# Kernel optimization log

Hardware: AMD Instinct MI355X
Metric: run time of the kernel (lower is better)

## Reference

```python
import jax, jax.numpy as jnp
import numpy as np
from jax import lax

# ---- Haar (db1) wavelet filters, matching create_wavelet_filter ----
_S2 = float(1.0 / np.sqrt(2.0))
_dec_lo = np.array([_S2, _S2], np.float32)    # pywt dec_lo reversed (symmetric)
_dec_hi = np.array([_S2, -_S2], np.float32)   # pywt dec_hi [-s,s] reversed
_rec_lo = np.array([_S2, _S2], np.float32)    # pywt rec_lo flipped (symmetric)
_rec_hi = np.array([-_S2, _S2], np.float32)   # pywt rec_hi [s,-s] flipped

def _outer(a, b):  # torch: a.unsqueeze(0) * b.unsqueeze(1) -> [i,j] = a[j]*b[i]
    return b[:, None] * a[None, :]

DEC = jnp.asarray(np.stack([_outer(_dec_lo, _dec_lo), _outer(_dec_lo, _dec_hi),
                            _outer(_dec_hi, _dec_lo), _outer(_dec_hi, _dec_hi)]))  # [4,2,2]
REC = jnp.asarray(np.stack([_outer(_rec_lo, _rec_lo), _outer(_rec_lo, _rec_hi),
                            _outer(_rec_hi, _rec_lo), _outer(_rec_hi, _rec_hi)]))  # [4,2,2]

BN_EPS = 1e-5

def mish(x):
    return x * jnp.tanh(jax.nn.softplus(x))

def silu(x):
    return x * jax.nn.sigmoid(x)

def bn(x, g, b):  # eval-mode BatchNorm2d with running_mean=0, running_var=1
    return x * (g / jnp.sqrt(1.0 + BN_EPS))[None, :, None, None] + b[None, :, None, None]

def dwconv(x, w, pad):  # depthwise conv, w: [C,1,k,k]
    return lax.conv_general_dilated(x, w, (1, 1), [(pad, pad), (pad, pad)],
                                    feature_group_count=x.shape[1],
                                    dimension_numbers=('NCHW', 'OIHW', 'NCHW'))

def dyn_dwconv(x, ew, gw):
    # DynamicConv2d (depthwise experts). ew: [E,C,1,k,k], gw: [E,C]
    gates = jax.nn.softmax(x.mean((2, 3)) @ gw.T, axis=-1)  # [B,E]
    k = ew.shape[-1]
    outs = jnp.stack([dwconv(x, ew[e], k // 2) for e in range(ew.shape[0])], 1)  # [B,E,C,H,W]
    return jnp.einsum('be,bechw->bchw', gates, outs)

def local_branch(x, ew, gw, bn1g, bn1b, pw, bn2g, bn2b):
    # DWConv2d_BN_ReLU: dynamic dwconv -> BN -> Mish -> depthwise 1x1 (per-channel scale) -> BN
    y = mish(bn(dyn_dwconv(x, ew, gw), bn1g, bn1b))
    y = y * pw[None, :, None, None]
    return bn(y, bn2g, bn2b)

def sel_scan(u, xw, dtw, dtb, Alog, Dp):
    # u: [B,L,D]; xw: [R+2N,D]; dtw: [D,R]; dtb: [D]; Alog: [D,N]; Dp: [D]
    R = dtw.shape[1]
    N = Alog.shape[1]
    xdbl = jnp.einsum('bld,ed->ble', u, xw)
    dt, Bm, Cm = xdbl[..., :R], xdbl[..., R:R + N], xdbl[..., R + N:]
    delta = jax.nn.softplus(jnp.einsum('blr,dr->bld', dt, dtw) + dtb)  # [B,L,D]
    A = -jnp.exp(Alog)                                                  # [D,N]
    a = jnp.exp(delta[..., None] * A)                                   # [B,L,D,N]
    b = delta[..., None] * Bm[:, :, None, :] * u[..., None]             # [B,L,D,N]
    def comb(c1, c2):
        a1, b1 = c1
        a2, b2 = c2
        return a1 * a2, a2 * b1 + b2
    _, h = lax.associative_scan(comb, (a, b), axis=1)                    # h_t = a_t h_{t-1} + b_t
    return jnp.einsum('bldn,bln->bld', h, Cm) + Dp * u

def ss2d(x, in_w, cw, cb, xpw, dtw, dtb, Alog, Dp, ow):
    # SS2D (d_state=1, k_group=2, channel_first): in_proj -> dwconv+silu -> 2-direction
    # selective scan -> gate with silu(z) -> out_proj.
    B, C, H, W = x.shape
    xz = jnp.einsum('oc,bchw->bohw', in_w, x)
    d = in_w.shape[0] // 2
    xi, z = xz[:, :d], xz[:, d:]
    xc = silu(dwconv(xi, cw, 1) + cb[None, :, None, None])
    u0 = xc.reshape(B, d, H * W).transpose(0, 2, 1)                       # row-major scan
    u1 = xc.transpose(0, 1, 3, 2).reshape(B, d, H * W).transpose(0, 2, 1)  # col-major scan
    y0 = sel_scan(u0, xpw[0], dtw[0], dtb[0], Alog[0], Dp[0])
    y1 = sel_scan(u1, xpw[1], dtw[1], dtb[1], Alog[1], Dp[1])
    y0 = y0.transpose(0, 2, 1).reshape(B, d, H, W)
    y1 = y1.transpose(0, 2, 1).reshape(B, d, W, H).transpose(0, 1, 3, 2)
    y = (y0 + y1) * silu(z)
    return jnp.einsum('oc,bchw->bohw', ow, y)

def mbwt(x, wav_w, wav_b, wav_scale, base_scale,
         ss_in_w, ss_conv_w, ss_conv_b, ss_xproj_w, ss_dt_w, ss_dt_b, ss_A_log, ss_D, ss_out_w):
    # MBWTConv2d, wt_levels=1, H/W even. Haar WT (2x2 stride 2) == block reshape + einsum.
    B, C, H, W = x.shape
    xr = x.reshape(B, C, H // 2, 2, W // 2, 2)
    wt = jnp.einsum('bchpwq,kpq->bckhw', xr, DEC)                  # [B,C,4,h,w]
    tag = wt.reshape(B, 4 * C, H // 2, W // 2)
    tag = dwconv(tag, wav_w, wav_w.shape[-1] // 2) + wav_b[None, :, None, None]
    tag = (tag * wav_scale).reshape(B, C, 4, H // 2, W // 2)
    # inverse Haar WT (conv_transpose 2x2 stride 2, groups=C)
    up = jnp.einsum('bckhw,kpq->bchpwq', tag, REC).reshape(B, C, H, W)
    g = ss2d(x, ss_in_w, ss_conv_w, ss_conv_b, ss_xproj_w, ss_dt_w, ss_dt_b, ss_A_log, ss_D, ss_out_w)
    return base_scale * g + up


def setup_inputs() -> dict:
    key = jax.random.key(0)
    ks = iter(jax.random.split(key, 64))
    B, DIM, H, W = 16, 256, 64, 64
    Cg = Cl = 64
    d = {'x': jax.random.normal(next(ks), (B, DIM, H, W), jnp.float32)}
    for j, k in enumerate((3, 5, 7)):
        p = f'l{j}_'
        d[p + 'ew'] = jax.random.normal(next(ks), (4, Cl, 1, k, k), jnp.float32) * 0.1
        d[p + 'gw'] = jax.random.normal(next(ks), (4, Cl), jnp.float32) * 0.1
        d[p + 'bn1g'] = jnp.ones((Cl,), jnp.float32)
        d[p + 'bn1b'] = jnp.zeros((Cl,), jnp.float32)
        d[p + 'pw'] = jax.random.normal(next(ks), (Cl,), jnp.float32) * 0.2
        d[p + 'bn2g'] = jnp.ones((Cl,), jnp.float32)
        d[p + 'bn2b'] = jnp.zeros((Cl,), jnp.float32)
    d['wav_w'] = jax.random.normal(next(ks), (4 * Cg, 1, 3, 3), jnp.float32) * 0.1
    d['wav_b'] = jnp.zeros((4 * Cg,), jnp.float32)
    d['wav_scale'] = jnp.full((1, 4 * Cg, 1, 1), 0.1, jnp.float32)
    d['base_scale'] = jnp.ones((1, Cg, 1, 1), jnp.float32)
    dm, R, N, K = Cg, 4, 1, 2  # d_inner, dt_rank, d_state, k_group
    d['ss_in_w'] = jax.random.normal(next(ks), (2 * dm, Cg), jnp.float32) * float(1 / np.sqrt(Cg))
    d['ss_conv_w'] = jax.random.normal(next(ks), (dm, 1, 3, 3), jnp.float32) * 0.1
    d['ss_conv_b'] = jnp.zeros((dm,), jnp.float32)
    d['ss_xproj_w'] = jax.random.normal(next(ks), (K, R + 2 * N, dm), jnp.float32) * float(1 / np.sqrt(dm))
    d['ss_dt_w'] = jax.random.normal(next(ks), (K, dm, R), jnp.float32) * float(1 / np.sqrt(R))
    d['ss_dt_b'] = jnp.full((K, dm), -2.0, jnp.float32)
    d['ss_A_log'] = jnp.zeros((K, dm, N), jnp.float32)
    d['ss_D'] = jnp.ones((K, dm), jnp.float32)
    d['ss_out_w'] = jax.random.normal(next(ks), (Cg, dm), jnp.float32) * float(1 / np.sqrt(dm))
    return d


def reference(x,
              l0_ew, l0_gw, l0_bn1g, l0_bn1b, l0_pw, l0_bn2g, l0_bn2b,
              l1_ew, l1_gw, l1_bn1g, l1_bn1b, l1_pw, l1_bn2g, l1_bn2b,
              l2_ew, l2_gw, l2_bn1g, l2_bn1b, l2_pw, l2_bn2g, l2_bn2b,
              wav_w, wav_b, wav_scale, base_scale,
              ss_in_w, ss_conv_w, ss_conv_b, ss_xproj_w, ss_dt_w, ss_dt_b, ss_A_log, ss_D, ss_out_w):
    Cg, Cl = 64, 64
    xg, xl, xi = x[:, :Cg], x[:, Cg:Cg + Cl], x[:, Cg + Cl:]
    yl = (local_branch(xl, l0_ew, l0_gw, l0_bn1g, l0_bn1b, l0_pw, l0_bn2g, l0_bn2b)
          + local_branch(xl, l1_ew, l1_gw, l1_bn1g, l1_bn1b, l1_pw, l1_bn2g, l1_bn2b)
          + local_branch(xl, l2_ew, l2_gw, l2_bn1g, l2_bn1b, l2_pw, l2_bn2g, l2_bn2b))
    yg = mbwt(xg, wav_w, wav_b, wav_scale, base_scale,
              ss_in_w, ss_conv_w, ss_conv_b, ss_xproj_w, ss_dt_w, ss_dt_b, ss_A_log, ss_D, ss_out_w)
    return jnp.concatenate([yg, yl, xi], axis=1)
```

## Files before the change

### kernel.cpp

```cpp
#include <hip/hip_runtime.h>
#include <math.h>

static constexpr int NB   = 16;
static constexpr int DIM  = 256;
static constexpr int CG   = 64;
static constexpr int HH   = 64;
static constexpr int WW   = 64;
static constexpr int HW   = HH * WW;

__device__ __forceinline__ float mish_fast(float x) {
    float t = __expf(fminf(x, 20.f));
    float p = __builtin_fmaf(t, t, t + t);
    return x * p * __builtin_amdgcn_rcpf(p + 2.f);
}
__device__ __forceinline__ float silu_f(float x) {
    return x * __builtin_amdgcn_rcpf(1.f + __expf(-x));
}
__device__ __forceinline__ float softplus_fast(float x) {
    return fmaxf(x, 0.f) + __logf(1.f + __expf(-fabsf(x)));
}

__global__ __launch_bounds__(256) void k_stage1(
    const float* __restrict__ x,
    const float* __restrict__ wav_w, const float* __restrict__ wav_b,
    const float* __restrict__ wav_scale,
    float* __restrict__ up, float* __restrict__ mean,
    const float* __restrict__ in_w,
    float* __restrict__ xi, float* __restrict__ z) {
    __shared__ float smem[8640];
    int bid = blockIdx.x;
    int tid = threadIdx.x;

    if (bid < 1024) {
        int c = bid & 63, b = bid >> 6;
        float* xs  = smem;
        float* wtb = smem + 4160;
        float* red = smem + 8384;
        const float* xp = x + ((size_t)b * DIM + c) * HW;
        for (int i = tid; i < HW; i += 256) xs[(i >> 6) * 65 + (i & 63)] = xp[i];
        {
            const float* lp = x + ((size_t)b * DIM + 64 + c) * HW;
            float s = 0.f;
            for (int i = tid; i < HW; i += 256) s += lp[i];
            red[tid] = s;
            __syncthreads();
            for (int o = 128; o > 0; o >>= 1) {
                if (tid < o) red[tid] += red[tid + o];
                __syncthreads();
            }
            if (tid == 0) mean[b * 64 + c] = red[0] * (1.f / HW);
        }
        for (int i = tid; i < 1024; i += 256) {
            int h = i >> 5, w = i & 31;
            float a  = xs[(2 * h) * 65 + 2 * w],     bb = xs[(2 * h) * 65 + 2 * w + 1];
            float cc = xs[(2 * h + 1) * 65 + 2 * w], dd = xs[(2 * h + 1) * 65 + 2 * w + 1];
            wtb[0 * 1056 + h * 33 + w] = 0.5f * (a + bb + cc + dd);
            wtb[1 * 1056 + h * 33 + w] = 0.5f * (a + bb - cc - dd);
            wtb[2 * 1056 + h * 33 + w] = 0.5f * (a - bb + cc - dd);
            wtb[3 * 1056 + h * 33 + w] = 0.5f * (a - bb - cc + dd);
        }
        __syncthreads();
        float wk[4][9], tb[4];
#pragma unroll
        for (int k = 0; k < 4; ++k) {
            int ch = c * 4 + k;
            float sc = wav_scale[ch];
#pragma unroll
            for (int j = 0; j < 9; ++j) wk[k][j] = wav_w[ch * 9 + j] * sc;
            tb[k] = wav_b[ch] * sc;
        }
        float* upp = up + ((size_t)b * CG + c) * HW;
        for (int i = tid; i < 1024; i += 256) {
            int h = i >> 5, w = i & 31;
            float tg[4];
#pragma unroll
            for (int k = 0; k < 4; ++k) {
                float s = tb[k];
#pragma unroll
                for (int dy = -1; dy <= 1; ++dy) {
                    int hh = h + dy;
                    if (hh < 0 || hh >= 32) continue;
#pragma unroll
                    for (int dx = -1; dx <= 1; ++dx) {
                        int wx = w + dx;
                        if (wx < 0 || wx >= 32) continue;
                        s = fmaf(wtb[k * 1056 + hh * 33 + wx], wk[k][(dy + 1) * 3 + (dx + 1)], s);
                    }
                }
                tg[k] = s;
            }
            float u00 = 0.5f * (tg[0] - tg[1] - tg[2] + tg[3]);
            float u01 = 0.5f * (tg[0] - tg[1] + tg[2] - tg[3]);
            float u10 = 0.5f * (tg[0] + tg[1] - tg[2] - tg[3]);
            float u11 = 0.5f * (tg[0] + tg[1] + tg[2] + tg[3]);
            upp[(2 * h) * 64 + 2 * w]         = u00;
            upp[(2 * h) * 64 + 2 * w + 1]     = u01;
            upp[(2 * h + 1) * 64 + 2 * w]     = u10;
            upp[(2 * h + 1) * 64 + 2 * w + 1] = u11;
        }
    } else {
        int id2 = bid - 1024;
        int h0 = (id2 & 31) * 2;
        int b  = id2 >> 5;
        float* xs = smem;
        float* wt = smem + 4096;

        float acc[8][8];
#pragma unroll
        for (int i = 0; i < 8; ++i)
#pragma unroll
            for (int j = 0; j < 8; ++j) acc[i][j] = 0.f;

        int o0 = (tid >> 4) * 8;
        int p0 = (tid & 15) * 8;

        for (int ko = 0; ko < 64; ko += 32) {
            if (ko) __syncthreads();
            {
                int s = tid;
#pragma unroll
                for (int it = 0; it < 4; ++it, s += 256) {
                    int c = s >> 5, p4 = (s & 31) * 4;
                    float4 v = *(const float4*)(x + ((size_t)b * DIM + ko + c) * HW + h0 * 64 + p4);
                    *(float4*)(xs + c * 128 + p4) = v;
                }
            }
            {
                int s = tid;
#pragma unroll
                for (int it = 0; it < 4; ++it, s += 256) {
                    int o = s >> 3, c0 = (s & 7) * 4;
                    float4 v = *(const float4*)(in_w + o * 64 + ko + c0);
                    wt[(c0 + 0) * 128 + o] = v.x;
                    wt[(c0 + 1) * 128 + o] = v.y;
                    wt[(c0 + 2) * 128 + o] = v.z;
                    wt[(c0 + 3) * 128 + o] = v.w;
                }
            }
            __syncthreads();
#pragma unroll 4
            for (int c = 0; c < 32; ++c) {
                float xv[8], wv[8];
                *(float4*)(xv)     = *(const float4*)(xs + c * 128 + p0);
                *(float4*)(xv + 4) = *(const float4*)(xs + c * 128 + p0 + 4);
                *(float4*)(wv)     = *(const float4*)(wt + c * 128 + o0);
                *(float4*)(wv + 4) = *(const float4*)(wt + c * 128 + o0 + 4);
#pragma unroll
                for (int i = 0; i < 8; ++i)
#pragma unroll
                    for (int j = 0; j < 8; ++j)
                        acc[i][j] = fmaf(wv[i], xv[j], acc[i][j]);
            }
        }

#pragma unroll
        for (int i = 0; i < 8; ++i) {
            int o = o0 + i;
            float* dst = (o < 64) ? (xi + ((size_t)b * 64 + o) * HW + h0 * 64)
                                  : (z + ((size_t)b * 64 + (o - 64)) * HW + h0 * 64);
            *(float4*)(dst + p0)     = make_float4(acc[i][0], acc[i][1], acc[i][2], acc[i][3]);
            *(float4*)(dst + p0 + 4) = make_float4(acc[i][4], acc[i][5], acc[i][6], acc[i][7]);
        }
    }
}

__global__ __launch_bounds__(256) void k_stage2(
    const float* __restrict__ xi,
    const float* __restrict__ cw, const float* __restrict__ cb,
    const float* __restrict__ xpw,
    float* __restrict__ xc, float4* __restrict__ proj4, float2* __restrict__ projBC,
    const float* __restrict__ mean,
    const float* __restrict__ ew3, const float* __restrict__ gw3, const float* __restrict__ g13,
    const float* __restrict__ ew5, const float* __restrict__ gw5, const float* __restrict__ g15,
    const float* __restrict__ ew7, const float* __restrict__ gw7, const float* __restrict__ g17,
    float* __restrict__ w3o, float* __restrict__ w5o, float* __restrict__ w7o) {
    __shared__ float smem[12608];
    int bid = blockIdx.x;
    int tid = threadIdx.x;

    if (bid < 512) {
        int h0 = (bid & 31) * 2;
        int b  = bid >> 5;
        float* xs  = smem;
        float* xcs = smem + 8448;

        int dir = tid >> 7;
        int px  = tid & 127;
        float acc0 = 0.f, acc1 = 0.f, acc2 = 0.f, acc3 = 0.f, acc4 = 0.f, acc5 = 0.f;

        int cl_c = tid >> 3;
        int p0_c = (tid & 7) * 16;
        int row_c = p0_c >> 6;
        int wb_c  = p0_c & 63;

        for (int ch0 = 0; ch0 < 64; ch0 += 32) {
            if (ch0) __syncthreads();
            {
                int s = tid;
#pragma unroll
                for (int it = 0; it < 8; ++it, s += 256) {
                    int c = s >> 6;
                    int rem = s & 63;
                    int r = rem >> 4, w4 = (rem & 15) * 4;
                    int gh = h0 - 1 + r;
                    float4 v = make_float4(0.f, 0.f, 0.f, 0.f);
                    if (gh >= 0 && gh < 64)
                        v = *(const float4*)(xi + ((size_t)b * 64 + ch0 + c) * HW + gh * 64 + w4);
                    float* dp = xs + c * 264 + r * 66 + 1 + w4;
                    dp[0] = v.x; dp[1] = v.y; dp[2] = v.z; dp[3] = v.w;
                }
                if (tid < 128) {
                    int cl = tid >> 2, r = tid & 3;
                    xs[cl * 264 + r * 66 + 0]  = 0.f;
                    xs[cl * 264 + r * 66 + 65] = 0.f;
                }
            }
            __syncthreads();

            {
                float wk[9];
#pragma unroll
                for (int j = 0; j < 9; ++j) wk[j] = cw[(ch0 + cl_c) * 9 + j];
                float bias = cb[ch0 + cl_c];
                float accr[16];
#pragma unroll
                for (int k = 0; k < 16; ++k) accr[k] = bias;
#pragma unroll
                for (int dy = 0; dy < 3; ++dy) {
                    const float* rp = xs + cl_c * 264 + (row_c + dy) * 66 + wb_c;
                    float r[18];
#pragma unroll
                    for (int q = 0; q < 18; ++q) r[q] = rp[q];
#pragma unroll
                    for (int k = 0; k < 16; ++k)
#pragma unroll
                        for (int dx = 0; dx < 3; ++dx)
                            accr[k] = fmaf(r[k + dx], wk[dy * 3 + dx], accr[k]);
                }
#pragma unroll
                for (int k = 0; k < 16; ++k)
                    xcs[cl_c * 130 + p0_c + k] = silu_f(accr[k]);
            }
            __syncthreads();

            {
                int s = tid;
#pragma unroll
                for (int it = 0; it < 4; ++it, s += 256) {
                    int c = s >> 5, pq = (s & 31) * 4;
                    const float* sp = xcs + c * 130 + pq;
                    *(float4*)(xc + ((size_t)b * 64 + ch0 + c) * HW + h0 * 64 + pq) =
                        make_float4(sp[0], sp[1], sp[2], sp[3]);
                }
            }
            {
                const float* wp = xpw + dir * 6 * 64 + ch0;
#pragma unroll 8
                for (int c = 0; c < 32; ++c) {
                    float xv = xcs[c * 130 + px];
                    acc0 = fmaf(xv, wp[0 * 64 + c], acc0);
                    acc1 = fmaf(xv, wp[1 * 64 + c], acc1);
                    acc2 = fmaf(xv, wp[2 * 64 + c], acc2);
                    acc3 = fmaf(xv, wp[3 * 64 + c], acc3);
                    acc4 = fmaf(xv, wp[4 * 64 + c], acc4);
                    acc5 = fmaf(xv, wp[5 * 64 + c], acc5);
                }
            }
        }

        int h = h0 + (px >> 6), w = px & 63;
        int l = (dir == 0) ? (h * 64 + w) : (w * 64 + h);
        size_t base = ((size_t)dir * NB + b) * HW + l;
        proj4[base]  = make_float4(acc0, acc1, acc2, acc3);
        projBC[base] = make_float2(acc4, acc5);
    } else {
        int b = bid - 512;
        int c = tid;
        float* m = smem;
        float* g = smem + 64;
        if (c < 64) m[c] = mean[b * 64 + c];
        __syncthreads();
        const float rs = rsqrtf(1.f + 1e-5f);

#define WEFF_SECT(GW, EW, G1, OUT, K2)                                        \
        {                                                                     \
            if (c < 4) {                                                      \
                float l = 0.f;                                                \
                for (int cc = 0; cc < 64; ++cc) l += m[cc] * GW[c * 64 + cc]; \
                g[c] = l;                                                     \
            }                                                                 \
            __syncthreads();                                                  \
            if (c == 0) {                                                     \
                float mx = fmaxf(fmaxf(g[0], g[1]), fmaxf(g[2], g[3]));       \
                float e0 = expf(g[0] - mx), e1 = expf(g[1] - mx);             \
                float e2 = expf(g[2] - mx), e3 = expf(g[3] - mx);             \
                float inv = 1.f / (e0 + e1 + e2 + e3);                        \
                g[0] = e0 * inv; g[1] = e1 * inv; g[2] = e2 * inv; g[3] = e3 * inv; \
            }                                                                 \
            __syncthreads();                                                  \
            if (c < 64) {                                                     \
                float g1s = G1[c] * rs;                                       \
                for (int kk = 0; kk < K2; ++kk) {                             \
                    float w = 0.f;                                            \
                    for (int e = 0; e < 4; ++e) w += g[e] * EW[(e * 64 + c) * K2 + kk]; \
                    OUT[(b * 64 + c) * K2 + kk] = w * g1s;                    \
                }                                                             \
            }                                                                 \
            __syncthreads();                                                  \
        }

        WEFF_SECT(gw3, ew3, g13, w3o, 9)
        WEFF_SECT(gw5, ew5, g15, w5o, 25)
        WEFF_SECT(gw7, ew7, g17, w7o, 49)
#undef WEFF_SECT
    }
}

__global__ __launch_bounds__(256) void k_scan2(const float* __restrict__ xc,
                                               const float4* __restrict__ proj4,
                                               const float2* __restrict__ projBC,
                                               const float* __restrict__ dt_w,
                                               const float* __restrict__ dt_b,
                                               const float* __restrict__ A_log,
                                               const float* __restrict__ Dp,
                                               const float* __restrict__ z,
                                               float* __restrict__ yz) {
    int wave = threadIdx.x >> 6;
    int lane = threadIdx.x & 63;
    int wid = blockIdx.x;
    int b = wid >> 6;
    int d = wid & 63;

    __shared__ float ut[64 * 65];
    __shared__ float al[4][1088];
    __shared__ float bl[4][1088];
    __shared__ float aggA[4], aggB[4];

    const float* uplane = xc + ((size_t)b * 64 + d) * HW;
    const float4* up4 = (const float4*)uplane;
#pragma unroll
    for (int q = 0; q < 4; ++q) {
        int s = q * 256 + threadIdx.x;
        float4 v = up4[s];
        int r = s >> 4, c0 = (s & 15) * 4;
        float* p = ut + r * 65 + c0;
        p[0] = v.x; p[1] = v.y; p[2] = v.z; p[3] = v.w;
    }
    __syncthreads();

    int ch = wave;
    float* a_my = al[wave];
    float* b_my = bl[wave];
    float y0r[16];

    {
        float4 wv = *(const float4*)(dt_w + d * 4);
        float db = dt_b[d];
        float A = -__expf(A_log[d]);
        float Dv = Dp[d];
        const float4* p4 = proj4 + (size_t)b * HW;
        const float2* pBC = projBC + (size_t)b * HW;

        float uv[16], cm[16];
#pragma unroll
        for (int j = 0; j < 16; ++j) {
            int el = j * 64 + lane;
            int e  = ch * 1024 + el;
            float4 t4 = p4[e];
            float2 t2 = pBC[e];
            float u = ut[(ch * 16 + j) * 65 + lane];
            uv[j] = u; cm[j] = t2.y;
            float pre = fmaf(t4.x, wv.x, fmaf(t4.y, wv.y,
                        fmaf(t4.z, wv.z, fmaf(t4.w, wv.w, db))));
            float delta = softplus_fast(pre);
            float aj = __expf(delta * A);
            float bj = delta * t2.x * u;
            int idx = (el >> 4) * 17 + (el & 15);
            a_my[idx] = aj;
            b_my[idx] = bj;
        }
        __builtin_amdgcn_wave_barrier();

        float a[16], bb[16];
#pragma unroll
        for (int j = 0; j < 16; ++j) {
            a[j]  = a_my[lane * 17 + j];
            bb[j] = b_my[lane * 17 + j];
        }
        float As = 1.f, Bs = 0.f;
#pragma unroll
        for (int j = 0; j < 16; ++j) { Bs = fmaf(a[j], Bs, bb[j]); As *= a[j]; }
        float Ai = As, Bi = Bs;
#pragma unroll
        for (int off = 1; off < 64; off <<= 1) {
            float ap = __shfl_up(Ai, (unsigned)off, 64);
            float bp = __shfl_up(Bi, (unsigned)off, 64);
            if (lane >= off) { Bi = fmaf(Ai, bp, Bi); Ai *= ap; }
        }
        if (lane == 63) { aggA[wave] = Ai; aggB[wave] = Bi; }
        __syncthreads();
        float carry = 0.f;
        for (int k = 0; k < wave; ++k) carry = fmaf(aggA[k], carry, aggB[k]);
        float ap1 = __shfl_up(Ai, 1, 64);
        float bp1 = __shfl_up(Bi, 1, 64);
        float h = (lane == 0) ? carry : fmaf(ap1, carry, bp1);
#pragma unroll
        for (int j = 0; j < 16; ++j) {
            h = fmaf(a[j], h, bb[j]);
            a_my[lane * 17 + j] = h;
        }
        __builtin_amdgcn_wave_barrier();
#pragma unroll
        for (int j = 0; j < 16; ++j) {
            int el = j * 64 + lane;
            float hv = a_my[(el >> 4) * 17 + (el & 15)];
            y0r[j] = fmaf(hv, cm[j], Dv * uv[j]);
        }
    }
    __syncthreads();

    {
        int pd = 64 + d;
        float4 wv = *(const float4*)(dt_w + pd * 4);
        float db = dt_b[pd];
        float A = -__expf(A_log[pd]);
        float Dv = Dp[pd];
        const float4* p4 = proj4 + ((size_t)NB + b) * HW;
        const float2* pBC = projBC + ((size_t)NB + b) * HW;

        float uv[16], cm[16];
#pragma unroll
        for (int j = 0; j < 16; ++j) {
            int el = j * 64 + lane;
            int e  = ch * 1024 + el;
            float4 t4 = p4[e];
            float2 t2 = pBC[e];
            float u = ut[lane * 65 + (ch * 16 + j)];
            uv[j] = u; cm[j] = t2.y;
            float pre = fmaf(t4.x, wv.x, fmaf(t4.y, wv.y,
                        fmaf(t4.z, wv.z, fmaf(t4.w, wv.w, db))));
            float delta = softplus_fast(pre);
            float aj = __expf(delta * A);
            float bj = delta * t2.x * u;
            int idx = (el >> 4) * 17 + (el & 15);
            a_my[idx] = aj;
            b_my[idx] = bj;
        }
        __builtin_amdgcn_wave_barrier();

        float a[16], bb[16];
#pragma unroll
        for (int j = 0; j < 16; ++j) {
            a[j]  = a_my[lane * 17 + j];
            bb[j] = b_my[lane * 17 + j];
        }
        float As = 1.f, Bs = 0.f;
#pragma unroll
        for (int j = 0; j < 16; ++j) { Bs = fmaf(a[j], Bs, bb[j]); As *= a[j]; }
        float Ai = As, Bi = Bs;
#pragma unroll
        for (int off = 1; off < 64; off <<= 1) {
            float ap = __shfl_up(Ai, (unsigned)off, 64);
            float bp = __shfl_up(Bi, (unsigned)off, 64);
            if (lane >= off) { Bi = fmaf(Ai, bp, Bi); Ai *= ap; }
        }
        if (lane == 63) { aggA[wave] = Ai; aggB[wave] = Bi; }
        __syncthreads();
        float carry = 0.f;
        for (int k = 0; k < wave; ++k) carry = fmaf(aggA[k], carry, aggB[k]);
        float ap1 = __shfl_up(Ai, 1, 64);
        float bp1 = __shfl_up(Bi, 1, 64);
        float h = (lane == 0) ? carry : fmaf(ap1, carry, bp1);
#pragma unroll
        for (int j = 0; j < 16; ++j) {
            h = fmaf(a[j], h, bb[j]);
            a_my[lane * 17 + j] = h;
        }
        __builtin_amdgcn_wave_barrier();
#pragma unroll
        for (int j = 0; j < 16; ++j) {
            int el = j * 64 + lane;
            float hv = a_my[(el >> 4) * 17 + (el & 15)];
            ut[lane * 65 + (ch * 16 + j)] = fmaf(hv, cm[j], Dv * uv[j]);
        }
    }
    __syncthreads();

    const float* zp = z + ((size_t)b * 64 + d) * HW;
    float* yp = yz + ((size_t)b * 64 + d) * HW;
#pragma unroll
    for (int j = 0; j < 16; ++j) {
        int e = ch * 1024 + j * 64 + lane;
        float y1v = ut[(ch * 16 + j) * 65 + lane];
        float zz = zp[e];
        yp[e] = (y0r[j] + y1v) * silu_f(zz);
    }
}

__global__ __launch_bounds__(256) void k_stage4(
    const float* __restrict__ x,
    const float* __restrict__ w3, const float* __restrict__ w5, const float* __restrict__ w7,
    const float* __restrict__ b1_0, const float* __restrict__ pw0,
    const float* __restrict__ g2_0, const float* __restrict__ b2_0,
    const float* __restrict__ b1_1, const float* __restrict__ pw1,
    const float* __restrict__ g2_1, const float* __restrict__ b2_1,
    const float* __restrict__ b1_2, const float* __restrict__ pw2,
    const float* __restrict__ g2_2, const float* __restrict__ b2_2,
    const float* __restrict__ yz, const float* __restrict__ ow,
    const float* __restrict__ base_scale, const float* __restrict__ up,
    float* __restrict__ out) {
    __shared__ float smem[6144];
    int bid = blockIdx.x;
    int tid = threadIdx.x;

    if (bid < 4096) {
        int tile = bid & 3;
        int c = (bid >> 2) & 63;
        int b = bid >> 8;
        int oy = (tile >> 1) * 32, ox = (tile & 1) * 32;
        float* t = smem;
        const float* xp = x + ((size_t)b * DIM + 64 + c) * HW;
        for (int i = tid; i < 38 * 38; i += 256) {
            int r = i / 38, cc = i % 38;
            int yy = r - 3 + oy, xx = cc - 3 + ox;
            t[r * 40 + cc] = (yy >= 0 && yy < 64 && xx >= 0 && xx < 64) ? xp[yy * 64 + xx] : 0.f;
        }
        {
            const float4* x4 = (const float4*)x;
            float4* o4 = (float4*)out;
            int base = bid * 512;
#pragma unroll
            for (int it = 0; it < 2; ++it) {
                int idx = base + it * 256 + tid;
                int bb = idx >> 17;
                int r  = idx & 131071;
                int gi = bb * 262144 + 131072 + r;
                o4[gi] = x4[gi];
            }
        }
        const float* w3p = w3 + (b * 64 + c) * 9;
        const float* w5p = w5 + (b * 64 + c) * 25;
        const float* w7p = w7 + (b * 64 + c) * 49;
        float W3r[9], W5r[25], W7r[49];
#pragma unroll
        for (int j = 0; j < 9; ++j)  W3r[j] = w3p[j];
#pragma unroll
        for (int j = 0; j < 25; ++j) W5r[j] = w5p[j];
#pragma unroll
        for (int j = 0; j < 49; ++j) W7r[j] = w7p[j];
        __syncthreads();

        const float rs = rsqrtf(1.f + 1e-5f);
        float bb1a = b1_0[c], bb1b = b1_1[c], bb1c = b1_2[c];
        float ssa = pw0[c] * g2_0[c] * rs, ssb = pw1[c] * g2_1[c] * rs, ssc = pw2[c] * g2_2[c] * rs;
        float bb2a = b2_0[c], bb2b = b2_1[c], bb2c = b2_2[c];

        int y  = tid >> 3;
        int x0 = (tid & 7) * 4;

        float a3[4] = {0.f, 0.f, 0.f, 0.f};
        float a5[4] = {0.f, 0.f, 0.f, 0.f};
        float a7[4] = {0.f, 0.f, 0.f, 0.f};

#pragma unroll
        for (int dy = 0; dy < 7; ++dy) {
            const float4* rp = (const float4*)(t + (y + dy) * 40 + x0);
            float4 q0 = rp[0], q1 = rp[1], q2 = rp[2];
            float r[12] = {q0.x, q0.y, q0.z, q0.w, q1.x, q1.y, q1.z, q1.w,
                           q2.x, q2.y, q2.z, q2.w};
#pragma unroll
            for (int k = 0; k < 4; ++k)
#pragma unroll
                for (int dx = 0; dx < 7; ++dx)
                    a7[k] = fmaf(r[k + dx], W7r[dy * 7 + dx], a7[k]);
            if (dy >= 1 && dy <= 5) {
                int ey = dy - 1;
#pragma unroll
                for (int k = 0; k < 4; ++k)
#pragma unroll
                    for (int dx = 0; dx < 5; ++dx)
                        a5[k] = fmaf(r[k + 1 + dx], W5r[ey * 5 + dx], a5[k]);
            }
            if (dy >= 2 && dy <= 4) {
                int ey = dy - 2;
#pragma unroll
                for (int k = 0; k < 4; ++k)
#pragma unroll
                    for (int dx = 0; dx < 3; ++dx)
                        a3[k] = fmaf(r[k + 2 + dx], W3r[ey * 3 + dx], a3[k]);
            }
        }

        float4 res;
        float* rr = (float*)&res;
#pragma unroll
        for (int k = 0; k < 4; ++k) {
            rr[k] = mish_fast(a3[k] + bb1a) * ssa + bb2a
                  + mish_fast(a5[k] + bb1b) * ssb + bb2b
                  + mish_fast(a7[k] + bb1c) * ssc + bb2c;
        }
        float* op = out + ((size_t)b * DIM + 64 + c) * HW;
        *(float4*)(op + (oy + y) * 64 + ox + x0) = res;
    } else {
        int id2 = bid - 4096;
        int h0 = (id2 & 31) * 2;
        int b  = id2 >> 5;
        float* yv = smem;
        float* wt = smem + 4096;

        float acc[8][4];
#pragma unroll
        for (int i = 0; i < 8; ++i)
#pragma unroll
            for (int j = 0; j < 4; ++j) acc[i][j] = 0.f;

        int o0 = (tid >> 5) * 8;
        int p0 = (tid & 31) * 4;

        for (int ko = 0; ko < 64; ko += 32) {
            if (ko) __syncthreads();
            {
                int s = tid;
#pragma unroll
                for (int it = 0; it < 4; ++it, s += 256) {
                    int c = s >> 5, p4 = (s & 31) * 4;
                    size_t idx = ((size_t)b * 64 + ko + c) * HW + h0 * 64 + p4;
                    *(float4*)(yv + c * 128 + p4) = *(const float4*)(yz + idx);
                }
            }
            {
                int s = tid;
#pragma unroll
                for (int it = 0; it < 2; ++it, s += 256) {
                    int o = s >> 3, c0 = (s & 7) * 4;
                    float4 v = *(const float4*)(ow + o * 64 + ko + c0);
                    wt[(c0 + 0) * 64 + o] = v.x;
                    wt[(c0 + 1) * 64 + o] = v.y;
                    wt[(c0 + 2) * 64 + o] = v.z;
                    wt[(c0 + 3) * 64 + o] = v.w;
                }
            }
            __syncthreads();
#pragma unroll 4
            for (int c = 0; c < 32; ++c) {
                float wv[8], xv[4];
                *(float4*)(wv)     = *(const float4*)(wt + c * 64 + o0);
                *(float4*)(wv + 4) = *(const float4*)(wt + c * 64 + o0 + 4);
                *(float4*)(xv)     = *(const float4*)(yv + c * 128 + p0);
#pragma unroll
                for (int i = 0; i < 8; ++i)
#pragma unroll
                    for (int j = 0; j < 4; ++j)
                        acc[i][j] = fmaf(wv[i], xv[j], acc[i][j]);
            }
        }

#pragma unroll
        for (int i = 0; i < 8; ++i) {
            int o = o0 + i;
            float bs = base_scale[o];
            float4 u = *(const float4*)(up + ((size_t)b * 64 + o) * HW + h0 * 64 + p0);
            float4 r = make_float4(fmaf(bs, acc[i][0], u.x),
                                   fmaf(bs, acc[i][1], u.y),
                                   fmaf(bs, acc[i][2], u.z),
                                   fmaf(bs, acc[i][3], u.w));
            *(float4*)(out + ((size_t)b * DIM + o) * HW + h0 * 64 + p0) = r;
        }
    }
}

extern "C" void kernel_launch(void* const* d_in, const int* in_sizes, int n_in,
                              void* d_out, int out_size, void* d_ws, size_t ws_size,
                              hipStream_t stream) {
    (void)in_sizes; (void)n_in; (void)out_size; (void)ws_size;
    const float* x = (const float*)d_in[0];
    float* out = (float*)d_out;
    float* ws = (float*)d_ws;

    const size_t IMG = (size_t)NB * 64 * HW;
    float* buf_xi   = ws;
    float* buf_z    = ws + IMG;
    float* buf_xc   = ws + 2 * IMG;
    float* buf_up   = ws + 3 * IMG;
    float* buf_p4   = ws + 4 * IMG;
    float* buf_pBC  = buf_p4 + (size_t)4 * 2 * NB * HW;
    float* buf_mean = buf_pBC + (size_t)2 * 2 * NB * HW;
    float* buf_w3   = buf_mean + 1024;
    float* buf_w5   = buf_w3 + 16 * 64 * 9;
    float* buf_w7   = buf_w5 + 16 * 64 * 25;

    k_stage1<<<1536, 256, 0, stream>>>(x,
        (const float*)d_in[22], (const float*)d_in[23], (const float*)d_in[24],
        buf_up, buf_mean,
        (const float*)d_in[26], buf_xi, buf_z);

    k_stage2<<<528, 256, 0, stream>>>(buf_xi,
        (const float*)d_in[27], (const float*)d_in[28], (const float*)d_in[29],
        buf_xc, (float4*)buf_p4, (float2*)buf_pBC,
        buf_mean,
        (const float*)d_in[1],  (const float*)d_in[2],  (const float*)d_in[3],
        (const float*)d_in[8],  (const float*)d_in[9],  (const float*)d_in[10],
        (const float*)d_in[15], (const float*)d_in[16], (const float*)d_in[17],
        buf_w3, buf_w5, buf_w7);

    k_scan2<<<1024, 256, 0, stream>>>(buf_xc, (const float4*)buf_p4, (const float2*)buf_pBC,
        (const float*)d_in[30], (const float*)d_in[31],
        (const float*)d_in[32], (const float*)d_in[33],
        buf_z, buf_xi);

    k_stage4<<<4608, 256, 0, stream>>>(x, buf_w3, buf_w5, buf_w7,
        (const float*)d_in[4],  (const float*)d_in[5],  (const float*)d_in[6],  (const float*)d_in[7],
        (const float*)d_in[11], (const float*)d_in[12], (const float*)d_in[13], (const float*)d_in[14],
        (const float*)d_in[18], (const float*)d_in[19], (const float*)d_in[20], (const float*)d_in[21],
        buf_xi, (const float*)d_in[34], (const float*)d_in[25], buf_up, out);
}
```

Before: 126.4 us.

## Interleave heterogeneous block types and vectorize wavelet stage loads/stores

Stage1 and stage4 now interleave their two block roles (wavelet/conv vs GEMM-style projection) across the grid instead of running them as contiguous ranges. The aim is to balance the load across CUs and overlap memory-bound and compute-bound work. Stage1 also drops the full-image shared staging and computes the Haar transform directly from float4 global loads. The mean reduction and the upsampled stores are vectorized, and shared memory use goes down. The risks are the changed block-index mapping and the assumption that the launch grid sizes match the new 3:2 and 9:8 ratios.

```diff
diff --git a/kernel.cpp b/kernel.cpp
--- a/kernel.cpp
+++ b/kernel.cpp
@@ -27,21 +27,24 @@
     float* __restrict__ up, float* __restrict__ mean,
     const float* __restrict__ in_w,
     float* __restrict__ xi, float* __restrict__ z) {
-    __shared__ float smem[8640];
+    __shared__ float smem[8192];
     int bid = blockIdx.x;
     int tid = threadIdx.x;
 
-    if (bid < 1024) {
-        int c = bid & 63, b = bid >> 6;
-        float* xs  = smem;
-        float* wtb = smem + 4160;
-        float* red = smem + 8384;
+    if (bid % 3 != 2) {
+        int aid = (bid / 3) * 2 + (bid % 3);
+        int c = aid & 63, b = aid >> 6;
+        float* wtb = smem;
+        float* red = smem + 4352;
         const float* xp = x + ((size_t)b * DIM + c) * HW;
-        for (int i = tid; i < HW; i += 256) xs[(i >> 6) * 65 + (i & 63)] = xp[i];
+
         {
-            const float* lp = x + ((size_t)b * DIM + 64 + c) * HW;
+            const float4* lp4 = (const float4*)(x + ((size_t)b * DIM + 64 + c) * HW);
             float s = 0.f;
-            for (int i = tid; i < HW; i += 256) s += lp[i];
+            for (int i = tid; i < 1024; i += 256) {
+                float4 v = lp4[i];
+                s += (v.x + v.y) + (v.z + v.w);
+            }
             red[tid] = s;
             __syncthreads();
             for (int o = 128; o > 0; o >>= 1) {
@@ -50,16 +53,27 @@
             }
             if (tid == 0) mean[b * 64 + c] = red[0] * (1.f / HW);
         }
-        for (int i = tid; i < 1024; i += 256) {
-            int h = i >> 5, w = i & 31;
-            float a  = xs[(2 * h) * 65 + 2 * w],     bb = xs[(2 * h) * 65 + 2 * w + 1];
-            float cc = xs[(2 * h + 1) * 65 + 2 * w], dd = xs[(2 * h + 1) * 65 + 2 * w + 1];
-            wtb[0 * 1056 + h * 33 + w] = 0.5f * (a + bb + cc + dd);
-            wtb[1 * 1056 + h * 33 + w] = 0.5f * (a + bb - cc - dd);
-            wtb[2 * 1056 + h * 33 + w] = 0.5f * (a - bb + cc - dd);
-            wtb[3 * 1056 + h * 33 + w] = 0.5f * (a - bb - cc + dd);
+
+#pragma unroll
+        for (int it = 0; it < 2; ++it) {
+            int p = tid + it * 256;
+            int h = p >> 4, w2 = p & 15;
+            float4 top = *(const float4*)(xp + (2 * h) * 64 + 4 * w2);
+            float4 bot = *(const float4*)(xp + (2 * h + 1) * 64 + 4 * w2);
+            float a0 = top.x, b0 = top.y, c0q = bot.x, d0 = bot.y;
+            float a1 = top.z, b1 = top.w, c1q = bot.z, d1 = bot.w;
+            int base0 = h * 34 + 2 * w2;
+            *(float2*)(wtb + 0 * 1088 + base0) =
+                make_float2(0.5f * (a0 + b0 + c0q + d0), 0.5f * (a1 + b1 + c1q + d1));
+            *(float2*)(wtb + 1 * 1088 + base0) =
+                make_float2(0.5f * (a0 + b0 - c0q - d0), 0.5f * (a1 + b1 - c1q - d1));
+            *(float2*)(wtb + 2 * 1088 + base0) =
+                make_float2(0.5f * (a0 - b0 + c0q - d0), 0.5f * (a1 - b1 + c1q - d1));
+            *(float2*)(wtb + 3 * 1088 + base0) =
+                make_float2(0.5f * (a0 - b0 - c0q + d0), 0.5f * (a1 - b1 - c1q + d1));
         }
         __syncthreads();
+
         float wk[4][9], tb[4];
 #pragma unroll
         for (int k = 0; k < 4; ++k) {
@@ -84,7 +98,7 @@
                     for (int dx = -1; dx <= 1; ++dx) {
                         int wx = w + dx;
                         if (wx < 0 || wx >= 32) continue;
-                        s = fmaf(wtb[k * 1056 + hh * 33 + wx], wk[k][(dy + 1) * 3 + (dx + 1)], s);
+                        s = fmaf(wtb[k * 1088 + hh * 34 + wx], wk[k][(dy + 1) * 3 + (dx + 1)], s);
                     }
                 }
                 tg[k] = s;
@@ -93,13 +107,11 @@
             float u01 = 0.5f * (tg[0] - tg[1] + tg[2] - tg[3]);
             float u10 = 0.5f * (tg[0] + tg[1] - tg[2] - tg[3]);
             float u11 = 0.5f * (tg[0] + tg[1] + tg[2] + tg[3]);
-            upp[(2 * h) * 64 + 2 * w]         = u00;
-            upp[(2 * h) * 64 + 2 * w + 1]     = u01;
-            upp[(2 * h + 1) * 64 + 2 * w]     = u10;
-            upp[(2 * h + 1) * 64 + 2 * w + 1] = u11;
+            *(float2*)(upp + (2 * h) * 64 + 2 * w)     = make_float2(u00, u01);
+            *(float2*)(upp + (2 * h + 1) * 64 + 2 * w) = make_float2(u10, u11);
         }
     } else {
-        int id2 = bid - 1024;
+        int id2 = bid / 3;
         int h0 = (id2 & 31) * 2;
         int b  = id2 >> 5;
         float* xs = smem;
@@ -513,10 +525,11 @@
     int bid = blockIdx.x;
     int tid = threadIdx.x;
 
-    if (bid < 4096) {
-        int tile = bid & 3;
-        int c = (bid >> 2) & 63;
-        int b = bid >> 8;
+    if (bid % 9 != 8) {
+        int cidx = (bid / 9) * 8 + (bid % 9);
+        int tile = cidx & 3;
+        int c = (cidx >> 2) & 63;
+        int b = cidx >> 8;
         int oy = (tile >> 1) * 32, ox = (tile & 1) * 32;
         float* t = smem;
         const float* xp = x + ((size_t)b * DIM + 64 + c) * HW;
@@ -528,7 +541,7 @@
         {
             const float4* x4 = (const float4*)x;
             float4* o4 = (float4*)out;
-            int base = bid * 512;
+            int base = cidx * 512;
 #pragma unroll
             for (int it = 0; it < 2; ++it) {
                 int idx = base + it * 256 + tid;
@@ -602,7 +615,7 @@
         float* op = out + ((size_t)b * DIM + 64 + c) * HW;
         *(float4*)(op + (oy + y) * 64 + ox + x0) = res;
     } else {
-        int id2 = bid - 4096;
+        int id2 = bid / 9;
         int h0 = (id2 & 31) * 2;
         int b  = id2 >> 5;
         float* yv = smem;
```

Result: faster. 119.7 us (-5.3%).
